# Kernel tuning notes

Measured on AMD Instinct MI355X. Metric: run time of the kernel, lower is better.

## Reference

```python
import jax, jax.numpy as jnp
import numpy as np

N_BINS = 64  # number of piecewise-linear bins; bins vector has N_BINS+1 boundaries
BATCH = 1_000_000


def setup_inputs() -> dict:
    key = jax.random.key(0)
    kx, kb = jax.random.split(key)
    x = jax.random.normal(kx, (BATCH, 1), dtype=jnp.float32)
    # sorted quantile-like boundaries (what adapt() would produce via np.quantile)
    bins = jnp.sort(jax.random.normal(kb, (N_BINS + 1,), dtype=jnp.float32))
    return {"x": x, "bins": bins}


def reference(x, bins):
    # x: [B, 1]; bins: [n_bins+1] sorted boundaries (lookup_table keys 0..n_bins)
    n_bins = bins.shape[0] - 1
    b_lo = bins[:-1]            # boundary[i-1] for bin i=1..n_bins -> [n_bins]
    b_hi = bins[1:]             # boundary[i]                      -> [n_bins]
    idx = jnp.arange(n_bins)    # i-1 in the original loop (i runs 1..n_bins)

    # left_mask_i  = (x < b[i-1]) & (i > 1)        -> idx > 0
    # right_mask_i = (x >= b[i])  & (i < n_bins)   -> idx < n_bins-1
    left = (x < b_lo) & (idx > 0)                  # [B, n_bins]
    right = (x >= b_hi) & (idx < n_bins - 1)       # [B, n_bins]
    v = (x - b_lo) / (b_hi - b_lo)                 # [B, n_bins]

    other = left == right                          # both False inside the bin
    enc = jnp.where(left, 0.0, 1.0)
    enc = jnp.where(other, v, enc)
    return enc.reshape(-1, 1, n_bins)              # [B, 1, n_bins]
```

## Files before the change

kernel.cpp:

```cpp
#include <hip/hip_runtime.h>
#include <float.h>

#define NB 64

typedef float vfloat4 __attribute__((ext_vector_type(4)));

__global__ __launch_bounds__(256) void ple_kernel(const float* __restrict__ x,
                                                  const float* __restrict__ bins,
                                                  float* __restrict__ out,
                                                  unsigned total4) {
    __shared__ __align__(16) float s_rinv[NB];
    __shared__ __align__(16) float s_nlor[NB];
    __shared__ __align__(16) float s_cl[NB];
    __shared__ __align__(16) float s_ch[NB];

    const int tid = threadIdx.x;
    if (tid < NB) {
        const float lo   = bins[tid];
        const float hi   = bins[tid + 1];
        const float rinv = 1.0f / (hi - lo);
        s_rinv[tid] = rinv;
        s_nlor[tid] = -lo * rinv;
        s_cl[tid] = (tid == 0)      ? -FLT_MAX : 0.0f;
        s_ch[tid] = (tid == NB - 1) ?  FLT_MAX : 1.0f;
    }
    __syncthreads();

    const int j4 = (tid & 15) << 2;
    const vfloat4 rinv4 = *(const vfloat4*)&s_rinv[j4];
    const vfloat4 nlor4 = *(const vfloat4*)&s_nlor[j4];
    const vfloat4 cl4   = *(const vfloat4*)&s_cl[j4];
    const vfloat4 ch4   = *(const vfloat4*)&s_ch[j4];

    const unsigned step = (unsigned)gridDim.x << 10;
    unsigned base = ((unsigned)blockIdx.x << 10) + (unsigned)tid;

    float xv[4];
#pragma unroll
    for (int k = 0; k < 4; ++k) {
        const unsigned t = base + (unsigned)(k << 8);
        xv[k] = (t < total4) ? x[t >> 4] : 0.0f;
    }

    while (base < total4) {
        const unsigned nbase = base + step;

        float xn[4];
#pragma unroll
        for (int k = 0; k < 4; ++k) {
            const unsigned t = nbase + (unsigned)(k << 8);
            xn[k] = (t < total4) ? x[t >> 4] : 0.0f;
        }

#pragma unroll
        for (int k = 0; k < 4; ++k) {
            const unsigned t = base + (unsigned)(k << 8);
            vfloat4 r;
#pragma unroll
            for (int c = 0; c < 4; ++c) {
                const float v = fmaf(xv[k], rinv4[c], nlor4[c]);
                r[c] = fminf(fmaxf(v, cl4[c]), ch4[c]);
            }
            if (t < total4)
                *((vfloat4*)out + t) = r;
        }

#pragma unroll
        for (int k = 0; k < 4; ++k) xv[k] = xn[k];
        base = nbase;
    }
}

extern "C" void kernel_launch(void* const* d_in, const int* in_sizes, int n_in,
                              void* d_out, int out_size, void* d_ws, size_t ws_size,
                              hipStream_t stream) {
    const float* x    = (const float*)d_in[0];
    const float* bins = (const float*)d_in[1];
    float* out        = (float*)d_out;

    const int batch = in_sizes[0];
    const unsigned total4 = (unsigned)batch * (NB / 4);
    const unsigned chunks = (total4 + 1023) / 1024;
    const unsigned grid = chunks < 2048u ? chunks : 2048u;

    ple_kernel<<<(dim3)grid, 256, 0, stream>>>(x, bins, out, total4);
}
```

Baseline: 250.5 us.

## Assign contiguous chunk spans per block and deepen x prefetch to two iterations

Each block now owns a contiguous range of chunks instead of striding across the grid, with the grid sized to about 1024 blocks. The x loads are prefetched two iterations ahead with a three-stage register rotation. The aim is more sequential write streams per block and more loads in flight to hide memory latency. The cost is fewer blocks and more registers, and the last block may be uneven.

```diff
diff --git a/kernel.cpp b/kernel.cpp
--- a/kernel.cpp
+++ b/kernel.cpp
@@ -8,7 +8,8 @@
 __global__ __launch_bounds__(256) void ple_kernel(const float* __restrict__ x,
                                                   const float* __restrict__ bins,
                                                   float* __restrict__ out,
-                                                  unsigned total4) {
+                                                  unsigned total4,
+                                                  unsigned cpb) {
     __shared__ __align__(16) float s_rinv[NB];
     __shared__ __align__(16) float s_nlor[NB];
     __shared__ __align__(16) float s_cl[NB];
@@ -32,24 +33,31 @@
     const vfloat4 cl4   = *(const vfloat4*)&s_cl[j4];
     const vfloat4 ch4   = *(const vfloat4*)&s_ch[j4];
 
-    const unsigned step = (unsigned)gridDim.x << 10;
-    unsigned base = ((unsigned)blockIdx.x << 10) + (unsigned)tid;
+    const unsigned span = cpb << 10;
+    const unsigned startSlot = (unsigned)blockIdx.x * span;
+    if (startSlot >= total4) return;
+    unsigned blockEnd = startSlot + span;
+    if (blockEnd > total4) blockEnd = total4;
 
-    float xv[4];
+    unsigned base = startSlot + (unsigned)tid;
+
+    float xv[4], xn[4], xm[4];
 #pragma unroll
     for (int k = 0; k < 4; ++k) {
         const unsigned t = base + (unsigned)(k << 8);
         xv[k] = (t < total4) ? x[t >> 4] : 0.0f;
     }
+#pragma unroll
+    for (int k = 0; k < 4; ++k) {
+        const unsigned t = base + 1024u + (unsigned)(k << 8);
+        xn[k] = (t < total4) ? x[t >> 4] : 0.0f;
+    }
 
-    while (base < total4) {
-        const unsigned nbase = base + step;
-
-        float xn[4];
+    for (; base < blockEnd; base += 1024u) {
 #pragma unroll
         for (int k = 0; k < 4; ++k) {
-            const unsigned t = nbase + (unsigned)(k << 8);
-            xn[k] = (t < total4) ? x[t >> 4] : 0.0f;
+            const unsigned t = base + 2048u + (unsigned)(k << 8);
+            xm[k] = (t < total4) ? x[t >> 4] : 0.0f;
         }
 
 #pragma unroll
@@ -61,13 +69,12 @@
                 const float v = fmaf(xv[k], rinv4[c], nlor4[c]);
                 r[c] = fminf(fmaxf(v, cl4[c]), ch4[c]);
             }
-            if (t < total4)
+            if (t < blockEnd)
                 *((vfloat4*)out + t) = r;
         }
 
 #pragma unroll
-        for (int k = 0; k < 4; ++k) xv[k] = xn[k];
-        base = nbase;
+        for (int k = 0; k < 4; ++k) { xv[k] = xn[k]; xn[k] = xm[k]; }
     }
 }
 
@@ -80,8 +87,11 @@
 
     const int batch = in_sizes[0];
     const unsigned total4 = (unsigned)batch * (NB / 4);
-    const unsigned chunks = (total4 + 1023) / 1024;
-    const unsigned grid = chunks < 2048u ? chunks : 2048u;
+    const unsigned chunks = (total4 + 1023) >> 10;
 
-    ple_kernel<<<(dim3)grid, 256, 0, stream>>>(x, bins, out, total4);
+    unsigned cpb = (chunks + 1023) >> 10;
+    if (cpb == 0) cpb = 1;
+    const unsigned grid = (chunks + cpb - 1) / cpb;
+
+    ple_kernel<<<(dim3)grid, 256, 0, stream>>>(x, bins, out, total4, cpb);
 }
```

Result: no change. 250.8 us (+0.1%).
